# Performance work log

Hardware: AMD Instinct MI355X
Metric: run time of the kernel (lower is better)

## Reference

```python
import jax, jax.numpy as jnp
import numpy as np

SCALE_MIN, SCALE_MAX = 0.01, 10.0
LN_EPS = 1e-5

B, KIN, H, C = 32, 6144, 512, 5


def _kaiming_uniform(k, shape):
    # torch kaiming_uniform_(a=sqrt(5)) on (out,in): bound = 1/sqrt(fan_in)
    bound = 1.0 / np.sqrt(shape[1])
    return jax.random.uniform(k, shape, minval=-bound, maxval=bound, dtype=jnp.float32)


def setup_inputs() -> dict:
    key = jax.random.key(0)
    ks = jax.random.split(key, 16)
    inp = {"x": jax.random.normal(ks[0], (B, KIN), dtype=jnp.float32)}
    dims = [(H, KIN), (H, H), (H, H)]
    for i, (o, n) in enumerate(dims):
        inp[f"w{i}"] = _kaiming_uniform(ks[1 + 3 * i], (o, n))
        inp[f"t{i}"] = jax.random.uniform(ks[2 + 3 * i], (o, n), minval=-1.0, maxval=1.0, dtype=jnp.float32)
        inp[f"s{i}"] = jax.random.uniform(ks[3 + 3 * i], (o, n), minval=-2.0, maxval=0.0, dtype=jnp.float32)
        inp[f"g{i}"] = jnp.ones((o,), jnp.float32)
        inp[f"b{i}"] = jnp.zeros((o,), jnp.float32)
    inp["cw"] = _kaiming_uniform(ks[10], (C, H))
    cbound = 1.0 / np.sqrt(H)
    inp["cb"] = jax.random.uniform(ks[11], (C,), minval=-cbound, maxval=cbound, dtype=jnp.float32)
    return inp


def _wavelet_linear(h, w, t, sr):
    # h: (B, in), params: (out, in)
    scale = SCALE_MIN + (SCALE_MAX - SCALE_MIN) * jax.nn.sigmoid(sr)
    s = (h[:, None, :] - t[None]) / (scale[None] + 1e-8)  # (B, out, in)
    psi = (1.0 - s * s) * jnp.exp(-0.5 * s * s)  # mexican hat
    return jnp.einsum('boi,oi->bo', psi, w)


def _layer_norm(h, g, b):
    m = jnp.mean(h, axis=-1, keepdims=True)
    v = jnp.mean(jnp.square(h - m), axis=-1, keepdims=True)
    return (h - m) * jax.lax.rsqrt(v + LN_EPS) * g + b


def reference(x, w0, t0, s0, g0, b0, w1, t1, s1, g1, b1, w2, t2, s2, g2, b2, cw, cb):
    h = x
    for (w, t, sr, g, b) in [(w0, t0, s0, g0, b0), (w1, t1, s1, g1, b1), (w2, t2, s2, g2, b2)]:
        h = _layer_norm(jax.nn.silu(_wavelet_linear(h, w, t, sr)), g, b)
    return h @ cw.T + cb
```

## Files before the change

kernel.cpp:

```cpp
#include <hip/hip_runtime.h>

#define LN_EPS 1e-5f

template<int KIN, int BLOCK>
__global__ __launch_bounds__(BLOCK)
void wav_layer(const float* __restrict__ xin, const float* __restrict__ w,
               const float* __restrict__ t, const float* __restrict__ s,
               float* __restrict__ hout)
{
    constexpr int K4 = KIN / 4;
    const int o   = blockIdx.x;
    const int tid = threadIdx.x;

    const float4* __restrict__ x4 = (const float4*)xin;
    const float4* __restrict__ w4 = (const float4*)w + (size_t)o * K4;
    const float4* __restrict__ t4 = (const float4*)t + (size_t)o * K4;
    const float4* __restrict__ s4 = (const float4*)s + (size_t)o * K4;

    float acc[32];
#pragma unroll
    for (int b = 0; b < 32; ++b) acc[b] = 0.f;

    for (int i = tid; i < K4; i += BLOCK) {
        float4 wv = w4[i];
        float4 tv = t4[i];
        float4 sv = s4[i];
        float svv[4] = {sv.x, sv.y, sv.z, sv.w};
        float tvv[4] = {tv.x, tv.y, tv.z, tv.w};
        float wl[4]  = {wv.x, wv.y, wv.z, wv.w};
        float inv[4], ti[4];
#pragma unroll
        for (int j = 0; j < 4; ++j) {
            float sig   = __builtin_amdgcn_rcpf(1.f + __expf(-svv[j]));
            float scale = fmaf(9.99f, sig, 0.01f) + 1e-8f;
            inv[j] = __builtin_amdgcn_rcpf(scale);
            ti[j]  = tvv[j] * inv[j];
        }
#pragma unroll
        for (int b = 0; b < 32; ++b) {
            float4 xv = x4[(size_t)b * K4 + i];
            float xc[4] = {xv.x, xv.y, xv.z, xv.w};
#pragma unroll
            for (int j = 0; j < 4; ++j) {
                float u  = fmaf(xc[j], inv[j], -ti[j]);
                float u2 = u * u;
                float e  = __expf(-0.5f * u2);
                acc[b] = fmaf((1.f - u2) * e, wl[j], acc[b]);
            }
        }
    }

    __shared__ float red[(BLOCK / 64) * 32];
    const int lane = tid & 63;
    const int wid  = tid >> 6;
#pragma unroll
    for (int b = 0; b < 32; ++b) {
        float v = acc[b];
#pragma unroll
        for (int off = 32; off; off >>= 1) v += __shfl_down(v, off);
        if (lane == 0) red[wid * 32 + b] = v;
    }
    __syncthreads();
    if (tid < 32) {
        float v = 0.f;
#pragma unroll
        for (int k = 0; k < BLOCK / 64; ++k) v += red[k * 32 + tid];
        hout[tid * 512 + o] = v;
    }
}

__global__ __launch_bounds__(512)
void silu_ln(const float* __restrict__ hpre, const float* __restrict__ g,
             const float* __restrict__ bias, float* __restrict__ hout)
{
    const int b   = blockIdx.x;
    const int tid = threadIdx.x;
    float v = hpre[b * 512 + tid];
    float a = v * __builtin_amdgcn_rcpf(1.f + __expf(-v));

    float s1 = a, s2 = a * a;
#pragma unroll
    for (int off = 32; off; off >>= 1) {
        s1 += __shfl_down(s1, off);
        s2 += __shfl_down(s2, off);
    }
    __shared__ float r1[8], r2[8];
    const int lane = tid & 63, wid = tid >> 6;
    if (lane == 0) { r1[wid] = s1; r2[wid] = s2; }
    __syncthreads();
    float t1 = 0.f, t2 = 0.f;
#pragma unroll
    for (int k = 0; k < 8; ++k) { t1 += r1[k]; t2 += r2[k]; }
    float m   = t1 * (1.f / 512.f);
    float var = t2 * (1.f / 512.f) - m * m;
    float r   = __builtin_amdgcn_rsqf(var + LN_EPS);
    hout[b * 512 + tid] = (a - m) * r * g[tid] + bias[tid];
}

__global__ __launch_bounds__(64)
void classifier(const float* __restrict__ h, const float* __restrict__ cw,
                const float* __restrict__ cb, float* __restrict__ out)
{
    const int b = blockIdx.x, lane = threadIdx.x;
    float acc[5] = {0.f, 0.f, 0.f, 0.f, 0.f};
    for (int i = lane; i < 512; i += 64) {
        float hv = h[b * 512 + i];
#pragma unroll
        for (int c = 0; c < 5; ++c) acc[c] = fmaf(hv, cw[c * 512 + i], acc[c]);
    }
#pragma unroll
    for (int c = 0; c < 5; ++c) {
        float v = acc[c];
#pragma unroll
        for (int off = 32; off; off >>= 1) v += __shfl_down(v, off);
        if (lane == 0) out[b * 5 + c] = v + cb[c];
    }
}

extern "C" void kernel_launch(void* const* d_in, const int* in_sizes, int n_in,
                              void* d_out, int out_size, void* d_ws, size_t ws_size,
                              hipStream_t stream)
{
    const float* x  = (const float*)d_in[0];
    const float* w0 = (const float*)d_in[1];
    const float* t0 = (const float*)d_in[2];
    const float* s0 = (const float*)d_in[3];
    const float* g0 = (const float*)d_in[4];
    const float* b0 = (const float*)d_in[5];
    const float* w1 = (const float*)d_in[6];
    const float* t1 = (const float*)d_in[7];
    const float* s1 = (const float*)d_in[8];
    const float* g1 = (const float*)d_in[9];
    const float* b1 = (const float*)d_in[10];
    const float* w2 = (const float*)d_in[11];
    const float* t2 = (const float*)d_in[12];
    const float* s2 = (const float*)d_in[13];
    const float* g2 = (const float*)d_in[14];
    const float* b2 = (const float*)d_in[15];
    const float* cw = (const float*)d_in[16];
    const float* cb = (const float*)d_in[17];
    float* out = (float*)d_out;

    float* bufA = (float*)d_ws;
    float* bufB = bufA + 32 * 512;

    wav_layer<6144, 256><<<512, 256, 0, stream>>>(x,    w0, t0, s0, bufA);
    silu_ln<<<32, 512, 0, stream>>>(bufA, g0, b0, bufB);
    wav_layer<512, 128><<<512, 128, 0, stream>>>(bufB, w1, t1, s1, bufA);
    silu_ln<<<32, 512, 0, stream>>>(bufA, g1, b1, bufB);
    wav_layer<512, 128><<<512, 128, 0, stream>>>(bufB, w2, t2, s2, bufA);
    silu_ln<<<32, 512, 0, stream>>>(bufA, g2, b2, bufB);
    classifier<<<32, 64, 0, stream>>>(bufB, cw, cb, out);
}
```

Before: 205.6 us.

## Split first wavelet layer along K, transpose activations, and fuse classifier into final LN

Adds a transpose so activations are stored feature-major, letting each thread read contiguous float4 batches for its input index. The 6144-wide first layer is split across 6 K-chunks via a second grid dimension, and the partial sums are reduced inside the following SiLU+LayerNorm kernel. This raises block count and occupancy (launch bounds with min 4 blocks) for the dominant layer. It also switches exp to exp2 with prescaled constants, folds the weight into the polynomial FMA, and fuses the classifier into the last LayerNorm kernel. The costs are an extra transpose launch and extra partial-sum memory traffic.

```diff
diff --git a/kernel.cpp b/kernel.cpp
--- a/kernel.cpp
+++ b/kernel.cpp
@@ -1,58 +1,75 @@
 #include <hip/hip_runtime.h>
 
 #define LN_EPS 1e-5f
-
-template<int KIN, int BLOCK>
-__global__ __launch_bounds__(BLOCK)
-void wav_layer(const float* __restrict__ xin, const float* __restrict__ w,
+#define LOG2E 1.44269504f
+#define NHALF_LOG2E (-0.72134752f)
+
+#if __has_builtin(__builtin_amdgcn_exp2f)
+#define EXP2F(x) __builtin_amdgcn_exp2f(x)
+#else
+#define EXP2F(x) __expf((x) * 0.69314718f)
+#endif
+
+template<int KIN>
+__global__ __launch_bounds__(256)
+void transpose_x(const float* __restrict__ x, float* __restrict__ xT)
+{
+    int idx = blockIdx.x * 256 + threadIdx.x;
+    int i = idx >> 5, b = idx & 31;
+    xT[idx] = x[b * KIN + i];
+}
+
+template<int KIN, int BLOCK, int S>
+__global__ __launch_bounds__(BLOCK, 4)
+void wav_layer(const float* __restrict__ xT, const float* __restrict__ w,
                const float* __restrict__ t, const float* __restrict__ s,
-               float* __restrict__ hout)
+               float* __restrict__ part)
 {
     constexpr int K4 = KIN / 4;
+    constexpr int CHUNK = K4 / S;
     const int o   = blockIdx.x;
+    const int si  = blockIdx.y;
     const int tid = threadIdx.x;
 
-    const float4* __restrict__ x4 = (const float4*)xin;
     const float4* __restrict__ w4 = (const float4*)w + (size_t)o * K4;
     const float4* __restrict__ t4 = (const float4*)t + (size_t)o * K4;
     const float4* __restrict__ s4 = (const float4*)s + (size_t)o * K4;
+    const float4* __restrict__ x4 = (const float4*)xT;
 
     float acc[32];
 #pragma unroll
     for (int b = 0; b < 32; ++b) acc[b] = 0.f;
 
-    for (int i = tid; i < K4; i += BLOCK) {
-        float4 wv = w4[i];
-        float4 tv = t4[i];
-        float4 sv = s4[i];
-        float svv[4] = {sv.x, sv.y, sv.z, sv.w};
-        float tvv[4] = {tv.x, tv.y, tv.z, tv.w};
-        float wl[4]  = {wv.x, wv.y, wv.z, wv.w};
-        float inv[4], ti[4];
+    for (int i4 = si * CHUNK + tid; i4 < (si + 1) * CHUNK; i4 += BLOCK) {
+        float4 wv = w4[i4], tv = t4[i4], sv = s4[i4];
+        float wa[4] = {wv.x, wv.y, wv.z, wv.w};
+        float ta[4] = {tv.x, tv.y, tv.z, tv.w};
+        float sa[4] = {sv.x, sv.y, sv.z, sv.w};
+        const float4* __restrict__ xr = x4 + (size_t)i4 * 32;
 #pragma unroll
         for (int j = 0; j < 4; ++j) {
-            float sig   = __builtin_amdgcn_rcpf(1.f + __expf(-svv[j]));
-            float scale = fmaf(9.99f, sig, 0.01f) + 1e-8f;
-            inv[j] = __builtin_amdgcn_rcpf(scale);
-            ti[j]  = tvv[j] * inv[j];
-        }
-#pragma unroll
-        for (int b = 0; b < 32; ++b) {
-            float4 xv = x4[(size_t)b * K4 + i];
-            float xc[4] = {xv.x, xv.y, xv.z, xv.w};
-#pragma unroll
-            for (int j = 0; j < 4; ++j) {
-                float u  = fmaf(xc[j], inv[j], -ti[j]);
-                float u2 = u * u;
-                float e  = __expf(-0.5f * u2);
-                acc[b] = fmaf((1.f - u2) * e, wl[j], acc[b]);
+            float sig = __builtin_amdgcn_rcpf(1.f + EXP2F(-sa[j] * LOG2E));
+            float inv = __builtin_amdgcn_rcpf(fmaf(9.99f, sig, 0.01000001f));
+            float nti = -ta[j] * inv;
+            float wj  = wa[j];
+#pragma unroll
+            for (int b4 = 0; b4 < 8; ++b4) {
+                float4 xv = xr[j * 8 + b4];
+                float xa[4] = {xv.x, xv.y, xv.z, xv.w};
+#pragma unroll
+                for (int k = 0; k < 4; ++k) {
+                    float u  = fmaf(xa[k], inv, nti);
+                    float u2 = u * u;
+                    float e  = EXP2F(u2 * NHALF_LOG2E);
+                    float pw = fmaf(-wj, u2, wj);
+                    acc[b4 * 4 + k] = fmaf(pw, e, acc[b4 * 4 + k]);
+                }
             }
         }
     }
 
     __shared__ float red[(BLOCK / 64) * 32];
-    const int lane = tid & 63;
-    const int wid  = tid >> 6;
+    const int lane = tid & 63, wid = tid >> 6;
 #pragma unroll
     for (int b = 0; b < 32; ++b) {
         float v = acc[b];
@@ -65,18 +82,20 @@
         float v = 0.f;
 #pragma unroll
         for (int k = 0; k < BLOCK / 64; ++k) v += red[k * 32 + tid];
-        hout[tid * 512 + o] = v;
-    }
-}
-
+        part[(size_t)si * 16384 + tid * 512 + o] = v;
+    }
+}
+
+template<int S>
 __global__ __launch_bounds__(512)
-void silu_ln(const float* __restrict__ hpre, const float* __restrict__ g,
-             const float* __restrict__ bias, float* __restrict__ hout)
-{
-    const int b   = blockIdx.x;
-    const int tid = threadIdx.x;
-    float v = hpre[b * 512 + tid];
-    float a = v * __builtin_amdgcn_rcpf(1.f + __expf(-v));
+void silu_ln(const float* __restrict__ part, const float* __restrict__ g,
+             const float* __restrict__ bias, float* __restrict__ hT)
+{
+    const int b = blockIdx.x, tid = threadIdx.x;
+    float v = 0.f;
+#pragma unroll
+    for (int si = 0; si < S; ++si) v += part[(size_t)si * 16384 + b * 512 + tid];
+    float a = v * __builtin_amdgcn_rcpf(1.f + EXP2F(-v * LOG2E));
 
     float s1 = a, s2 = a * a;
 #pragma unroll
@@ -94,26 +113,53 @@
     float m   = t1 * (1.f / 512.f);
     float var = t2 * (1.f / 512.f) - m * m;
     float r   = __builtin_amdgcn_rsqf(var + LN_EPS);
-    hout[b * 512 + tid] = (a - m) * r * g[tid] + bias[tid];
-}
-
-__global__ __launch_bounds__(64)
-void classifier(const float* __restrict__ h, const float* __restrict__ cw,
-                const float* __restrict__ cb, float* __restrict__ out)
-{
-    const int b = blockIdx.x, lane = threadIdx.x;
-    float acc[5] = {0.f, 0.f, 0.f, 0.f, 0.f};
-    for (int i = lane; i < 512; i += 64) {
-        float hv = h[b * 512 + i];
-#pragma unroll
-        for (int c = 0; c < 5; ++c) acc[c] = fmaf(hv, cw[c * 512 + i], acc[c]);
-    }
+    hT[tid * 32 + b] = (a - m) * r * g[tid] + bias[tid];
+}
+
+template<int S>
+__global__ __launch_bounds__(512)
+void silu_ln_cls(const float* __restrict__ part, const float* __restrict__ g,
+                 const float* __restrict__ bias, const float* __restrict__ cw,
+                 const float* __restrict__ cb, float* __restrict__ out)
+{
+    const int b = blockIdx.x, tid = threadIdx.x;
+    float v = 0.f;
+#pragma unroll
+    for (int si = 0; si < S; ++si) v += part[(size_t)si * 16384 + b * 512 + tid];
+    float a = v * __builtin_amdgcn_rcpf(1.f + EXP2F(-v * LOG2E));
+
+    float s1 = a, s2 = a * a;
+#pragma unroll
+    for (int off = 32; off; off >>= 1) {
+        s1 += __shfl_down(s1, off);
+        s2 += __shfl_down(s2, off);
+    }
+    __shared__ float r1[8], r2[8];
+    const int lane = tid & 63, wid = tid >> 6;
+    if (lane == 0) { r1[wid] = s1; r2[wid] = s2; }
+    __syncthreads();
+    float t1 = 0.f, t2 = 0.f;
+#pragma unroll
+    for (int k = 0; k < 8; ++k) { t1 += r1[k]; t2 += r2[k]; }
+    float m   = t1 * (1.f / 512.f);
+    float var = t2 * (1.f / 512.f) - m * m;
+    float r   = __builtin_amdgcn_rsqf(var + LN_EPS);
+    float hl  = (a - m) * r * g[tid] + bias[tid];
+
+    __shared__ float cr[5][8];
 #pragma unroll
     for (int c = 0; c < 5; ++c) {
-        float v = acc[c];
-#pragma unroll
-        for (int off = 32; off; off >>= 1) v += __shfl_down(v, off);
-        if (lane == 0) out[b * 5 + c] = v + cb[c];
+        float pv = hl * cw[c * 512 + tid];
+#pragma unroll
+        for (int off = 32; off; off >>= 1) pv += __shfl_down(pv, off);
+        if (lane == 0) cr[c][wid] = pv;
+    }
+    __syncthreads();
+    if (tid < 5) {
+        float sum = 0.f;
+#pragma unroll
+        for (int k = 0; k < 8; ++k) sum += cr[tid][k];
+        out[b * 5 + tid] = sum + cb[tid];
     }
 }
 
@@ -141,14 +187,15 @@
     const float* cb = (const float*)d_in[17];
     float* out = (float*)d_out;
 
-    float* bufA = (float*)d_ws;
-    float* bufB = bufA + 32 * 512;
-
-    wav_layer<6144, 256><<<512, 256, 0, stream>>>(x,    w0, t0, s0, bufA);
-    silu_ln<<<32, 512, 0, stream>>>(bufA, g0, b0, bufB);
-    wav_layer<512, 128><<<512, 128, 0, stream>>>(bufB, w1, t1, s1, bufA);
-    silu_ln<<<32, 512, 0, stream>>>(bufA, g1, b1, bufB);
-    wav_layer<512, 128><<<512, 128, 0, stream>>>(bufB, w2, t2, s2, bufA);
-    silu_ln<<<32, 512, 0, stream>>>(bufA, g2, b2, bufB);
-    classifier<<<32, 64, 0, stream>>>(bufB, cw, cb, out);
-}
+    float* xT   = (float*)d_ws;
+    float* part = xT + 196608;
+    float* hT   = part + 6 * 16384;
+
+    transpose_x<6144><<<768, 256, 0, stream>>>(x, xT);
+    wav_layer<6144, 256, 6><<<dim3(512, 6), 256, 0, stream>>>(xT, w0, t0, s0, part);
+    silu_ln<6><<<32, 512, 0, stream>>>(part, g0, b0, hT);
+    wav_layer<512, 128, 1><<<dim3(512, 1), 128, 0, stream>>>(hT, w1, t1, s1, part);
+    silu_ln<1><<<32, 512, 0, stream>>>(part, g1, b1, hT);
+    wav_layer<512, 128, 1><<<dim3(512, 1), 128, 0, stream>>>(hT, w2, t2, s2, part);
+    silu_ln_cls<1><<<32, 512, 0, stream>>>(part, g2, b2, cw, cb, out);
+}
```

Result: no change. 204.0 us (-0.8%).
